# Optimization experiments

Measured on AMD Instinct MI355X. Metric: run time of the kernel, lower is better.

## Reference

```python
import jax, jax.numpy as jnp
import numpy as np

NEG_INF = -1e30  # stand-in for float('-inf'); avoids NaNs if a row is fully masked


def setup_inputs() -> dict:
    key = jax.random.key(0)
    k1, k2, k3, k4 = jax.random.split(key, 4)
    B, Q, K, D = 16, 2048, 2048, 64
    query = jax.random.normal(k1, (B, Q, D), dtype=jnp.float32)
    key_t = jax.random.normal(k2, (B, K, D), dtype=jnp.float32)
    value = jax.random.normal(k3, (B, K, D), dtype=jnp.float32)
    mask = jax.random.randint(k4, (B, Q, K), 0, 2).astype(jnp.bool_)
    return {"query": query, "key": key_t, "value": value, "mask": mask}


def reference(query, key, value, mask):
    d = query.shape[-1]
    # [B,Q,K] score matrix (naive attention, as in the original module)
    score = jnp.einsum('bqd,bkd->bqk', query, key) / jnp.sqrt(jnp.asarray(d, query.dtype))
    score = jnp.where(mask, NEG_INF, score)  # masked_fill(mask, -inf)
    attn = jax.nn.softmax(score, axis=-1)
    # dropout p=0.0 -> identity
    return jnp.einsum('bqk,bkd->bqd', attn, value)
```

## Files before the change

### kernel.cpp

```cpp
#include <hip/hip_runtime.h>


#define Bn   16
#define Qn   2048
#define Kseq 2048
#define Dn   64
#define QBLK 128
#define NEGF (-1e30f)

typedef __attribute__((ext_vector_type(4)))  short short4v;
typedef __attribute__((ext_vector_type(8)))  short short8;
typedef __attribute__((ext_vector_type(4)))  unsigned uint4v;
typedef __attribute__((ext_vector_type(16))) float f32x16;

static __device__ __forceinline__ short f2bf(float x) {
  union { float f; unsigned u; } un; un.f = x;
  unsigned r = un.u + 0x7FFFu + ((un.u >> 16) & 1u);
  return (short)(r >> 16);
}
static __device__ __forceinline__ unsigned pkbf(float lo, float hi) {
  unsigned r;
  asm("v_cvt_pk_bf16_f32 %0, %1, %2" : "=v"(r) : "v"(lo), "v"(hi));
  return r;
}
#if __has_builtin(__builtin_amdgcn_exp2f)
#define EXP2 __builtin_amdgcn_exp2f
#else
#define EXP2 exp2f
#endif
#define MFMA32 __builtin_amdgcn_mfma_f32_32x32x16_bf16

#define PREF_KV()                                                             \
  do {                                                                        \
    kst[0] = kp4[co0]; kst[1] = kp4[co1];                                     \
    kst[2] = kp4[co2]; kst[3] = kp4[co3];                                     \
    _Pragma("unroll")                                                         \
    for (int j2 = 0; j2 < 8; ++j2) vst[j2] = *(const float2*)(vp + j2 * 64);  \
    kp4 += 2048; vp += 8192;                                                  \
  } while (0)

#define PREF_M()                                                              \
  do {                                                                        \
    _Pragma("unroll")                                                         \
    for (int g = 0; g < 8; ++g) ma[g] = mp[2 * g];                            \
    mp += 32;                                                                 \
  } while (0)

#define WRITELDS()                                                            \
  do {                                                                        \
    _Pragma("unroll")                                                         \
    for (int i = 0; i < 4; ++i) {                                             \
      float4 a = kst[i]; short4v t;                                           \
      t[0] = f2bf(a.x); t[1] = f2bf(a.y); t[2] = f2bf(a.z); t[3] = f2bf(a.w); \
      *(short4v*)kdst[i] = t;                                                 \
    }                                                                         \
    short8 v0, v1;                                                            \
    _Pragma("unroll")                                                         \
    for (int j2 = 0; j2 < 8; ++j2) { v0[j2] = f2bf(vst[j2].x); v1[j2] = f2bf(vst[j2].y); } \
    *(short8*)vdst0 = v0; *(short8*)vdst1 = v1;                               \
  } while (0)

static __device__ __forceinline__ unsigned compress_mask(const int4* ma) {
  unsigned bits = 0;
#pragma unroll
  for (int g = 0; g < 8; ++g) {
    int4 m = ma[g];
    const int sh = ((g & 4) << 2) + ((g & 3) << 2);
    unsigned bsel = (m.x != 0 ? 1u : 0u) | (m.y != 0 ? 2u : 0u) |
                    (m.z != 0 ? 4u : 0u) | (m.w != 0 ? 8u : 0u);
    bits |= bsel << sh;
  }
  return bits;
}

#define COMPUTE()                                                             \
  do {                                                                        \
    f32x16 st0, st1;                                                          \
    _Pragma("unroll")                                                         \
    for (int i = 0; i < 16; ++i) { st0[i] = 0.f; st1[i] = 0.f; }              \
    _Pragma("unroll")                                                         \
    for (int s = 0; s < 4; ++s) {                                             \
      short8 kf = *(const short8*)(krd + ((32 * s + hh) ^ swz));              \
      st0 = MFMA32(kf, qf[s], st0, 0, 0, 0);                                  \
      short8 kg = *(const short8*)(krd + 4096 + ((32 * s + hh) ^ swz));       \
      st1 = MFMA32(kg, qf[s], st1, 0, 0, 0);                                  \
    }                                                                         \
    _Pragma("unroll")                                                         \
    for (int i = 0; i < 16; ++i) {                                            \
      st0[i] = (bits & (1u << i))       ? NEGF : st0[i];                      \
      st1[i] = (bits & (0x10000u << i)) ? NEGF : st1[i];                      \
    }                                                                         \
    float mx8[8];                                                             \
    _Pragma("unroll")                                                         \
    for (int i = 0; i < 8; ++i)                                               \
      mx8[i] = fmaxf(fmaxf(st0[i], st0[i+8]), fmaxf(st1[i], st1[i+8]));       \
    float mx = fmaxf(fmaxf(fmaxf(mx8[0],mx8[1]), fmaxf(mx8[2],mx8[3])),       \
                     fmaxf(fmaxf(mx8[4],mx8[5]), fmaxf(mx8[6],mx8[7])));      \
    mx = fmaxf(mx, __shfl_xor(mx, 32));                                       \
    if (!__all(mx <= mrun)) {                                                 \
      float mnew  = fmaxf(mrun, mx);                                          \
      float alpha = EXP2(mrun - mnew);                                        \
      lrun *= alpha;                                                          \
      _Pragma("unroll")                                                       \
      for (int i = 0; i < 16; ++i) { ot0[i] *= alpha; ot1[i] *= alpha; }      \
      mrun = mnew;                                                            \
    }                                                                         \
    _Pragma("unroll")                                                         \
    for (int i = 0; i < 16; ++i) {                                            \
      st0[i] = EXP2(st0[i] - mrun);                                           \
      st1[i] = EXP2(st1[i] - mrun);                                           \
    }                                                                         \
    float s8[8];                                                              \
    _Pragma("unroll")                                                         \
    for (int i = 0; i < 8; ++i) s8[i] = (st0[i]+st0[i+8]) + (st1[i]+st1[i+8]);\
    float lsum = ((s8[0]+s8[1]) + (s8[2]+s8[3])) +                            \
                 ((s8[4]+s8[5]) + (s8[6]+s8[7]));                             \
    lsum += __shfl_xor(lsum, 32);                                             \
    lrun += lsum;                                                             \
    short8 f0, f1, f2, f3;                                                    \
    {                                                                         \
      unsigned x0 = pkbf(st0[0],st0[1]),   x1 = pkbf(st0[2],st0[3]);          \
      unsigned y0 = pkbf(st0[4],st0[5]),   y1 = pkbf(st0[6],st0[7]);          \
      unsigned a0 = pkbf(st0[8],st0[9]),   a1 = pkbf(st0[10],st0[11]);        \
      unsigned b0 = pkbf(st0[12],st0[13]), b1 = pkbf(st0[14],st0[15]);        \
      unsigned sx0 = __shfl_xor(x0,32), sx1 = __shfl_xor(x1,32);              \
      unsigned sy0 = __shfl_xor(y0,32), sy1 = __shfl_xor(y1,32);              \
      unsigned sa0 = __shfl_xor(a0,32), sa1 = __shfl_xor(a1,32);              \
      unsigned sb0 = __shfl_xor(b0,32), sb1 = __shfl_xor(b1,32);              \
      uint4v u0 = { h ? sy0 : x0, h ? sy1 : x1, h ? y0 : sx0, h ? y1 : sx1 }; \
      uint4v u1 = { h ? sb0 : a0, h ? sb1 : a1, h ? b0 : sa0, h ? b1 : sa1 }; \
      f0 = __builtin_bit_cast(short8, u0);                                    \
      f1 = __builtin_bit_cast(short8, u1);                                    \
    }                                                                         \
    {                                                                         \
      unsigned x0 = pkbf(st1[0],st1[1]),   x1 = pkbf(st1[2],st1[3]);          \
      unsigned y0 = pkbf(st1[4],st1[5]),   y1 = pkbf(st1[6],st1[7]);          \
      unsigned a0 = pkbf(st1[8],st1[9]),   a1 = pkbf(st1[10],st1[11]);        \
      unsigned b0 = pkbf(st1[12],st1[13]), b1 = pkbf(st1[14],st1[15]);        \
      unsigned sx0 = __shfl_xor(x0,32), sx1 = __shfl_xor(x1,32);              \
      unsigned sy0 = __shfl_xor(y0,32), sy1 = __shfl_xor(y1,32);              \
      unsigned sa0 = __shfl_xor(a0,32), sa1 = __shfl_xor(a1,32);              \
      unsigned sb0 = __shfl_xor(b0,32), sb1 = __shfl_xor(b1,32);              \
      uint4v u2 = { h ? sy0 : x0, h ? sy1 : x1, h ? y0 : sx0, h ? y1 : sx1 }; \
      uint4v u3 = { h ? sb0 : a0, h ? sb1 : a1, h ? b0 : sa0, h ? b1 : sa1 }; \
      f2 = __builtin_bit_cast(short8, u2);                                    \
      f3 = __builtin_bit_cast(short8, u3);                                    \
    }                                                                         \
    _Pragma("unroll")                                                         \
    for (int s = 0; s < 4; ++s) {                                             \
      short8 pf = (s==0) ? f0 : (s==1) ? f1 : (s==2) ? f2 : f3;               \
      short8 va = *(const short8*)(vrd + ((32 * s + hh) ^ swz));              \
      ot0 = MFMA32(va, pf, ot0, 0, 0, 0);                                     \
      short8 vb = *(const short8*)(vrd + 4096 + ((32 * s + hh) ^ swz));       \
      ot1 = MFMA32(vb, pf, ot1, 0, 0, 0);                                     \
    }                                                                         \
  } while (0)

__launch_bounds__(512, 2)
__global__ void attn_fused(const float* __restrict__ Qg,
                           const float* __restrict__ Kg,
                           const float* __restrict__ Vg,
                           const int*   __restrict__ Mg,
                           float* __restrict__ Og) {
  __shared__ char ldsb[32768];

  const int tid  = threadIdx.x;
  const int lane = tid & 63;
  const int w    = tid >> 6;
  const int wq   = w & 3;
  const int grp  = w >> 2;
  const int l31  = lane & 31;
  const int h    = lane >> 5;
  const int hh   = h << 4;
  const int swz  = (l31 & 7) << 4;
  const int b    = blockIdx.y;
  const int qb   = blockIdx.x * QBLK;
  const int q    = qb + wq * 32 + l31;

  const float qscale = 0.18033688011112042f;
  const float* qp = Qg + ((size_t)(b * Qn + q)) * Dn + 8 * h;
  short8 qf[4];
#pragma unroll
  for (int s = 0; s < 4; ++s) {
    float4 a = *(const float4*)(qp + 16 * s);
    float4 c = *(const float4*)(qp + 16 * s + 4);
    short8 f;
    f[0]=f2bf(a.x*qscale); f[1]=f2bf(a.y*qscale); f[2]=f2bf(a.z*qscale); f[3]=f2bf(a.w*qscale);
    f[4]=f2bf(c.x*qscale); f[5]=f2bf(c.y*qscale); f[6]=f2bf(c.z*qscale); f[7]=f2bf(c.w*qscale);
    qf[s] = f;
  }

  const float4* kp4 = (const float4*)(Kg + (size_t)b * Kseq * Dn);
  const int co0 = tid, co1 = tid + 512, co2 = tid + 1024, co3 = tid + 1536;
  char* kdst[4];
#pragma unroll
  for (int i = 0; i < 4; ++i) {
    int c = tid + 512 * i;
    int row = c >> 4, col16 = c & 15;
    int tile = row >> 6, r = row & 63;
    kdst[i] = ldsb + tile * 8192 + r * 128 +
              (((col16 >> 1) << 4) ^ ((r & 7) << 4)) + ((col16 & 1) << 3);
  }

  const int uu = tid & 255, tileV = tid >> 8;
  const int d0 = (uu & 31) * 2, kv8 = (uu >> 5) * 8;
  const float* vp = Vg + ((size_t)b * Kseq + tileV * 64 + kv8) * Dn + d0;
  char* vdst0 = ldsb + 16384 + tileV * 8192 + d0 * 128 + ((kv8 * 2) ^ ((d0 & 7) << 4));
  char* vdst1 = ldsb + 16384 + tileV * 8192 + (d0 + 1) * 128 + ((kv8 * 2) ^ (((d0 + 1) & 7) << 4));

  const int4* mp = (const int4*)(Mg + ((size_t)(b * Qn + q)) * Kseq) + 16 * grp + h;

  const char* krd = ldsb + grp * 8192 + l31 * 128;
  const char* vrd = ldsb + 16384 + grp * 8192 + l31 * 128;

  f32x16 ot0, ot1;
#pragma unroll
  for (int i = 0; i < 16; ++i) { ot0[i] = 0.f; ot1[i] = 0.f; }
  float mrun = NEGF, lrun = 0.f;

  float4 kst[4];
  float2 vst[8];
  int4   ma[8];
  unsigned bits;

  PREF_KV();
  PREF_M();
  WRITELDS();
  bits = compress_mask(ma);
  __syncthreads();

#pragma unroll 1
  for (int j = 0; j < 16; ++j) {
    if (j < 15) { PREF_KV(); PREF_M(); }
    COMPUTE();
    if (j < 15) {
      bits = compress_mask(ma);
      __syncthreads();
      WRITELDS();
      __syncthreads();
    }
  }

  __syncthreads();

  float* lm = (float*)ldsb;
  float* ll = lm + 256;
  float* lo = ll + 256;
  const int s4 = wq * 64 + lane;
  if (grp == 1) {
    lm[s4] = mrun; ll[s4] = lrun;
#pragma unroll
    for (int i = 0; i < 16; ++i) lo[s4 * 20 + i] = ot0[i];
  }
  __syncthreads();
  float aA = 1.f, aB = 0.f;
  if (grp == 0) {
    float mB = lm[s4], lB = ll[s4];
    float ms = fmaxf(mrun, mB);
    aA = EXP2(mrun - ms); aB = EXP2(mB - ms);
    lrun = lrun * aA + lB * aB;
#pragma unroll
    for (int i = 0; i < 16; ++i) ot0[i] = ot0[i] * aA + lo[s4 * 20 + i] * aB;
  }
  __syncthreads();
  if (grp == 1) {
#pragma unroll
    for (int i = 0; i < 16; ++i) lo[s4 * 20 + i] = ot1[i];
  }
  __syncthreads();
  if (grp == 0) {
#pragma unroll
    for (int i = 0; i < 16; ++i) ot1[i] = ot1[i] * aA + lo[s4 * 20 + i] * aB;
    float inv = 1.0f / lrun;
    float* op = Og + ((size_t)(b * Qn + q)) * Dn;
#pragma unroll
    for (int g = 0; g < 4; ++g) {
      float4 o;
      o.x = ot0[4*g+0] * inv; o.y = ot0[4*g+1] * inv;
      o.z = ot0[4*g+2] * inv; o.w = ot0[4*g+3] * inv;
      *(float4*)(op + 8*g + 4*h) = o;
      o.x = ot1[4*g+0] * inv; o.y = ot1[4*g+1] * inv;
      o.z = ot1[4*g+2] * inv; o.w = ot1[4*g+3] * inv;
      *(float4*)(op + 32 + 8*g + 4*h) = o;
    }
  }
}

extern "C" void kernel_launch(void* const* d_in, const int* in_sizes, int n_in,
                              void* d_out, int out_size, void* d_ws, size_t ws_size,
                              hipStream_t stream) {
  const float* Q = (const float*)d_in[0];
  const float* K = (const float*)d_in[1];
  const float* V = (const float*)d_in[2];
  const int*   M = (const int*)d_in[3];
  float* O = (float*)d_out;
  dim3 grid(Qn / QBLK, Bn);
  attn_fused<<<grid, dim3(512), 0, stream>>>(Q, K, V, M, O);
}
```

Before: 409.2 us.

## Load mask cooperatively with coalesced reads and distribute bitmasks through LDS

Each thread previously read its own query row's mask with strided int4 loads. Now the block's threads load mask rows with contiguous 64-byte runs per thread and pack them into 16-bit bitmasks. These are written to an extra 2KB LDS region, and each lane reads back its packed bits inside the compute step. The goal is better-coalesced global reads of the dominant mask traffic, at the cost of more LDS use and an extra LDS read per tile.

```diff
diff --git a/kernel.cpp b/kernel.cpp
--- a/kernel.cpp
+++ b/kernel.cpp
@@ -42,8 +42,11 @@
 #define PREF_M()                                                              \
   do {                                                                        \
     _Pragma("unroll")                                                         \
-    for (int g = 0; g < 8; ++g) ma[g] = mp[2 * g];                            \
-    mp += 32;                                                                 \
+    for (int p = 0; p < 2; ++p)                                               \
+      _Pragma("unroll")                                                       \
+      for (int jj = 0; jj < 4; ++jj)                                          \
+        mld[p * 4 + jj] = mpp[p * 32768 + jj];                                \
+    mpp += 32;                                                                \
   } while (0)
 
 #define WRITELDS()                                                            \
@@ -58,23 +61,26 @@
     _Pragma("unroll")                                                         \
     for (int j2 = 0; j2 < 8; ++j2) { v0[j2] = f2bf(vst[j2].x); v1[j2] = f2bf(vst[j2].y); } \
     *(short8*)vdst0 = v0; *(short8*)vdst1 = v1;                               \
+    _Pragma("unroll")                                                         \
+    for (int p = 0; p < 2; ++p) {                                             \
+      unsigned v = 0;                                                         \
+      _Pragma("unroll")                                                       \
+      for (int jj = 0; jj < 4; ++jj) {                                        \
+        int4 m = mld[p * 4 + jj];                                             \
+        v |= (m.x != 0 ? 1u : 0u) << (jj * 4);                                \
+        v |= (m.y != 0 ? 2u : 0u) << (jj * 4);                                \
+        v |= (m.z != 0 ? 4u : 0u) << (jj * 4);                                \
+        v |= (m.w != 0 ? 8u : 0u) << (jj * 4);                                \
+      }                                                                       \
+      mwr[p * 512] = (unsigned short)v;                                       \
+    }                                                                         \
   } while (0)
-
-static __device__ __forceinline__ unsigned compress_mask(const int4* ma) {
-  unsigned bits = 0;
-#pragma unroll
-  for (int g = 0; g < 8; ++g) {
-    int4 m = ma[g];
-    const int sh = ((g & 4) << 2) + ((g & 3) << 2);
-    unsigned bsel = (m.x != 0 ? 1u : 0u) | (m.y != 0 ? 2u : 0u) |
-                    (m.z != 0 ? 4u : 0u) | (m.w != 0 ? 8u : 0u);
-    bits |= bsel << sh;
-  }
-  return bits;
-}
 
 #define COMPUTE()                                                             \
   do {                                                                        \
+    const uint2 mb = *(const uint2*)mrd;                                      \
+    const unsigned xh = mb.x >> (4 * h);                                      \
+    const unsigned yh = mb.y >> (4 * h);                                      \
     f32x16 st0, st1;                                                          \
     _Pragma("unroll")                                                         \
     for (int i = 0; i < 16; ++i) { st0[i] = 0.f; st1[i] = 0.f; }              \
@@ -87,8 +93,9 @@
     }                                                                         \
     _Pragma("unroll")                                                         \
     for (int i = 0; i < 16; ++i) {                                            \
-      st0[i] = (bits & (1u << i))       ? NEGF : st0[i];                      \
-      st1[i] = (bits & (0x10000u << i)) ? NEGF : st1[i];                      \
+      const int bi = 8 * (i >> 2) + (i & 3);                                  \
+      st0[i] = ((xh >> bi) & 1u) ? NEGF : st0[i];                             \
+      st1[i] = ((yh >> bi) & 1u) ? NEGF : st1[i];                             \
     }                                                                         \
     float mx8[8];                                                             \
     _Pragma("unroll")                                                         \
@@ -162,7 +169,7 @@
                            const float* __restrict__ Vg,
                            const int*   __restrict__ Mg,
                            float* __restrict__ Og) {
-  __shared__ char ldsb[32768];
+  __shared__ char ldsb[34816];
 
   const int tid  = threadIdx.x;
   const int lane = tid & 63;
@@ -208,7 +215,10 @@
   char* vdst0 = ldsb + 16384 + tileV * 8192 + d0 * 128 + ((kv8 * 2) ^ ((d0 & 7) << 4));
   char* vdst1 = ldsb + 16384 + tileV * 8192 + (d0 + 1) * 128 + ((kv8 * 2) ^ (((d0 + 1) & 7) << 4));
 
-  const int4* mp = (const int4*)(Mg + ((size_t)(b * Qn + q)) * Kseq) + 16 * grp + h;
+  const int4* mpp = (const int4*)(Mg + ((size_t)(b * Qn + qb + (tid >> 3))) * Kseq)
+                    + (tid & 7) * 4;
+  unsigned short* mwr = (unsigned short*)(ldsb + 32768) + (tid >> 3) * 8 + (tid & 7);
+  const char* mrd = ldsb + 32768 + (wq * 32 + l31) * 16 + grp * 8;
 
   const char* krd = ldsb + grp * 8192 + l31 * 128;
   const char* vrd = ldsb + 16384 + grp * 8192 + l31 * 128;
@@ -220,13 +230,11 @@
 
   float4 kst[4];
   float2 vst[8];
-  int4   ma[8];
-  unsigned bits;
+  int4   mld[8];
 
   PREF_KV();
   PREF_M();
   WRITELDS();
-  bits = compress_mask(ma);
   __syncthreads();
 
 #pragma unroll 1
@@ -234,7 +242,6 @@
     if (j < 15) { PREF_KV(); PREF_M(); }
     COMPUTE();
     if (j < 15) {
-      bits = compress_mask(ma);
       __syncthreads();
       WRITELDS();
       __syncthreads();
```

Result: faster. 380.4 us (-7.0%).
